# Optimization experiments

Measured on AMD Instinct MI355X. Metric: run time of the kernel, lower is better.

Reference implementation:

```python
import jax, jax.numpy as jnp
import numpy as np

B = 256          # batch
T = 256          # block_size (tril mask requires seq_len == 256)
E = 384          # n_embed
H = 6            # n_head
HS = E // H      # head_size = 64
EPS = 1e-5       # torch LayerNorm default


def layernorm(x, g, b):
    m = x.mean(-1, keepdims=True)
    v = x.var(-1, keepdims=True)  # population variance, matches torch LN
    return (x - m) * jax.lax.rsqrt(v + EPS) * g + b


def setup_inputs() -> dict:
    key = jax.random.key(0)
    ks = jax.random.split(key, 8)
    s = lambda i, shape: jax.random.normal(ks[i], shape, jnp.float32) * 0.02
    return {
        "x": jax.random.normal(ks[0], (B, T, E), jnp.float32),
        # per-head Q/K/V linears (bias=False) packed along output dim: [E, H*HS]
        "Wq": s(1, (E, E)), "Wk": s(2, (E, E)), "Wv": s(3, (E, E)),
        "Wo": s(4, (E, E)), "bo": jnp.zeros((E,), jnp.float32),
        "W1": s(5, (E, 4 * E)), "b1": jnp.zeros((4 * E,), jnp.float32),
        "W2": s(6, (4 * E, E)), "b2": jnp.zeros((E,), jnp.float32),
        "g1": jnp.ones((E,), jnp.float32), "be1": jnp.zeros((E,), jnp.float32),
        "g2": jnp.ones((E,), jnp.float32), "be2": jnp.zeros((E,), jnp.float32),
    }


def reference(x, Wq, Wk, Wv, Wo, bo, W1, b1, W2, b2, g1, be1, g2, be2):
    # Block.forward: ffwd(ln2(sa(ln1(x)) + x)) + x   (dropout = identity at eval)
    h = layernorm(x, g1, be1)                                  # [B,T,E]
    q = (h @ Wq).reshape(B, T, H, HS)
    k = (h @ Wk).reshape(B, T, H, HS)
    v = (h @ Wv).reshape(B, T, H, HS)
    wei = jnp.einsum('bqhd,bkhd->bhqk', q, k) * (HS ** -0.5)   # [B,H,T,T]
    mask = jnp.tril(jnp.ones((T, T), dtype=bool))
    wei = jnp.where(mask, wei, -jnp.inf)
    wei = jax.nn.softmax(wei, axis=-1)
    attn = jnp.einsum('bhqk,bkhd->bqhd', wei, v).reshape(B, T, E)
    sa = attn @ Wo + bo                                        # output projection
    y = sa + x                                                 # residual 1
    h2 = layernorm(y, g2, be2)
    ff = jax.nn.relu(h2 @ W1 + b1) @ W2 + b2                   # FFN
    return ff + x                                              # residual 2 (to x!)
```

## Files before the change

### kernel.cpp

```cpp
#include <hip/hip_runtime.h>
#include <hip/hip_bf16.h>

typedef unsigned short bfu;
typedef __attribute__((ext_vector_type(8))) short short8;
typedef __attribute__((ext_vector_type(4))) float f32x4;

__device__ __forceinline__ bfu f2bf(float f) {
  return __builtin_bit_cast(bfu, __float2bfloat16(f));
}

__device__ __forceinline__ void gld16(const void* g, void* l) {
  __builtin_amdgcn_global_load_lds(
      (const __attribute__((address_space(1))) void*)g,
      (__attribute__((address_space(3))) void*)l, 16, 0, 0);
}

__device__ __forceinline__ int swz8(int row, int sl) {
  return (row << 7) + (((sl ^ (row & 7)) & 7) << 4);
}

__device__ __forceinline__ int swz(int row, int slot) {
  const int unit = row >> 1;
  const int s8 = ((row & 1) << 2) | slot;
  return (unit << 7) + (((s8 ^ unit) & 7) << 4) + ((s8 >> 3) << 7);
}
__device__ __forceinline__ void unswz(int p, int& row, int& colel) {
  const int unit = p >> 7;
  const int s8 = ((p >> 4) & 7) ^ (unit & 7);
  row = (unit << 1) | (s8 >> 2);
  colel = (s8 & 3) << 3;
}

__global__ void transpose_all(const float* __restrict__ Wq, const float* __restrict__ Wk,
                              const float* __restrict__ Wv, const float* __restrict__ Wo,
                              const float* __restrict__ W1, const float* __restrict__ W2,
                              bfu* __restrict__ wqkvT, bfu* __restrict__ woT,
                              bfu* __restrict__ w1T, bfu* __restrict__ w2T) {
  int idx = blockIdx.x * 256 + threadIdx.x;
  if (idx < 4 * 147456) {
    int r = idx / 147456, i = idx - r * 147456;
    int k = i / 384, n = i - k * 384;
    const float* W = r == 0 ? Wq : r == 1 ? Wk : r == 2 ? Wv : Wo;
    bfu* dst = r < 3 ? wqkvT + r * 147456 : woT;
    dst[n * 384 + k] = f2bf(W[i]);
  } else if (idx < 4 * 147456 + 589824) {
    int i = idx - 4 * 147456;
    int k = i / 1536, n = i - k * 1536;
    w1T[n * 384 + k] = f2bf(W1[i]);
  } else if (idx < 4 * 147456 + 2 * 589824) {
    int i = idx - 4 * 147456 - 589824;
    int k = i / 384, n = i - k * 384;
    w2T[(size_t)n * 1536 + k] = f2bf(W2[i]);
  }
}

__launch_bounds__(256)
__global__ void ln_kernel(const float* __restrict__ in, const float* __restrict__ g,
                          const float* __restrict__ be, bfu* __restrict__ out) {
  const int wv = threadIdx.x >> 6, ln = threadIdx.x & 63;
  const size_t row = (size_t)blockIdx.x * 4 + wv;
  const float* p = in + row * 384;
  float v[6], s = 0.f, ss = 0.f;
#pragma unroll
  for (int i = 0; i < 6; i++) { v[i] = p[i * 64 + ln]; s += v[i]; ss += v[i] * v[i]; }
#pragma unroll
  for (int m = 1; m < 64; m <<= 1) { s += __shfl_xor(s, m); ss += __shfl_xor(ss, m); }
  const float mean = s * (1.f / 384.f);
  const float rs = rsqrtf(ss * (1.f / 384.f) - mean * mean + 1e-5f);
  bfu* q = out + row * 384;
#pragma unroll
  for (int i = 0; i < 6; i++) {
    const int c = i * 64 + ln;
    q[c] = f2bf((v[i] - mean) * rs * g[c] + be[c]);
  }
}

template <int BIAS, int RELU, int RES, int OUTBF>
__launch_bounds__(512)
__global__ void gemm8p(const bfu* __restrict__ A, const bfu* __restrict__ Bt,
                       const float* __restrict__ bias, const float* __restrict__ res,
                       void* __restrict__ Cout, int N, int K, int ntn) {
  __shared__ bfu sm[3][384 * 64];
  const int tid = threadIdx.x;
  const int wv = tid >> 6, ln = tid & 63;
  const int cpx = gridDim.x >> 3;
  const int wg = (blockIdx.x & 7) * cpx + (blockIdx.x >> 3);
  const int bm = wg / ntn, bn = wg - bm * ntn;
  const int m0 = bm << 8, n0 = bn << 7;
  const int wr = wv >> 1, wc = wv & 1;
  const int fr = ln & 15, fslot = ln >> 4;

  f32x4 acc[4][4];
#pragma unroll
  for (int i = 0; i < 4; i++)
#pragma unroll
    for (int j = 0; j < 4; j++) acc[i][j] = f32x4{0.f, 0.f, 0.f, 0.f};

  const int lr = ln >> 3;
  const int lslot = (ln & 7) ^ lr;

  auto stage = [&](int s, int kt) {
    char* smA = (char*)sm[s];
    char* smB = smA + 256 * 64 * 2;
    const int kcol = (kt << 6) + (lslot << 3);
#pragma unroll
    for (int i = 0; i < 4; ++i) {
      const int c = (wv << 2) + i;
      gld16(A + (size_t)(m0 + (c << 3) + lr) * K + kcol, smA + (c << 10));
    }
#pragma unroll
    for (int i = 0; i < 2; ++i) {
      const int c = (wv << 1) + i;
      gld16(Bt + (size_t)(n0 + (c << 3) + lr) * K + kcol, smB + (c << 10));
    }
  };

  const int nk = K >> 6;
  stage(0, 0);
  if (nk > 1) {
    stage(1, 1);
    asm volatile("s_waitcnt vmcnt(6)" ::: "memory");
  } else {
    asm volatile("s_waitcnt vmcnt(0)" ::: "memory");
  }
  __builtin_amdgcn_s_barrier();

  for (int kt = 0; kt < nk; ++kt) {
    const int s = kt - (kt / 3) * 3;
    const char* smA = (const char*)sm[s];
    const char* smB = smA + 256 * 64 * 2;
    if (kt + 2 < nk) stage((kt + 2) - ((kt + 2) / 3) * 3, kt + 2);
    short8 af[4], bf[4];
#pragma unroll
    for (int mi = 0; mi < 4; mi++)
      af[mi] = *(const short8*)(smA + swz8(wr * 64 + mi * 16 + fr, fslot));
#pragma unroll
    for (int ni = 0; ni < 4; ni++)
      bf[ni] = *(const short8*)(smB + swz8(wc * 64 + ni * 16 + fr, fslot));
    __builtin_amdgcn_s_barrier();
    asm volatile("s_waitcnt lgkmcnt(0)" ::: "memory");
    __builtin_amdgcn_sched_barrier(0);
    __builtin_amdgcn_s_setprio(1);
#pragma unroll
    for (int mi = 0; mi < 4; mi++)
#pragma unroll
      for (int ni = 0; ni < 4; ni++)
        acc[mi][ni] = __builtin_amdgcn_mfma_f32_16x16x32_bf16(af[mi], bf[ni], acc[mi][ni], 0, 0, 0);
    __builtin_amdgcn_s_setprio(0);
    __builtin_amdgcn_s_barrier();
#pragma unroll
    for (int mi = 0; mi < 4; mi++)
      af[mi] = *(const short8*)(smA + swz8(wr * 64 + mi * 16 + fr, 4 + fslot));
#pragma unroll
    for (int ni = 0; ni < 4; ni++)
      bf[ni] = *(const short8*)(smB + swz8(wc * 64 + ni * 16 + fr, 4 + fslot));
    __builtin_amdgcn_s_barrier();
    asm volatile("s_waitcnt lgkmcnt(0)" ::: "memory");
    __builtin_amdgcn_sched_barrier(0);
    __builtin_amdgcn_s_setprio(1);
#pragma unroll
    for (int mi = 0; mi < 4; mi++)
#pragma unroll
      for (int ni = 0; ni < 4; ni++)
        acc[mi][ni] = __builtin_amdgcn_mfma_f32_16x16x32_bf16(af[mi], bf[ni], acc[mi][ni], 0, 0, 0);
    __builtin_amdgcn_s_setprio(0);
    if (kt + 2 < nk)      asm volatile("s_waitcnt vmcnt(6)" ::: "memory");
    else if (kt + 1 < nk) asm volatile("s_waitcnt vmcnt(0)" ::: "memory");
    __builtin_amdgcn_s_barrier();
  }

  const int rq = (ln >> 4) << 2;
#pragma unroll
  for (int mi = 0; mi < 4; mi++) {
#pragma unroll
    for (int ni = 0; ni < 4; ni++) {
      const int row = m0 + wr * 64 + mi * 16 + rq;
      const int col = n0 + wc * 64 + ni * 16 + fr;
      float bv = 0.f;
      if (BIAS) bv = bias[col];
#pragma unroll
      for (int r = 0; r < 4; r++) {
        float v = acc[mi][ni][r] + bv;
        if (RELU) v = fmaxf(v, 0.f);
        const size_t idx = (size_t)(row + r) * N + col;
        if (RES) v += res[idx];
        if (OUTBF) ((bfu*)Cout)[idx] = f2bf(v);
        else       ((float*)Cout)[idx] = v;
      }
    }
  }
}

template <int LN>
__launch_bounds__(512)
__global__ void row_gemm(const bfu* __restrict__ A, const bfu* __restrict__ Bt,
                         const float* __restrict__ bias, const float* __restrict__ res,
                         const float* __restrict__ g, const float* __restrict__ be,
                         void* __restrict__ Cout, int K) {
  __shared__ bfu a_sm[4][128 * 32];
  __shared__ bfu b_sm[4][384 * 32];
  __shared__ float lnp[4][128][2];
  const int tid = threadIdx.x;
  const int wv = tid >> 6, ln = tid & 63;
  const int wr = wv >> 2, wc = wv & 3;
  const int fr = ln & 15, fslot = ln >> 4;
  const int m0 = blockIdx.x << 7;

  f32x4 acc[4][6];
#pragma unroll
  for (int i = 0; i < 4; i++)
#pragma unroll
    for (int j = 0; j < 6; j++) acc[i][j] = f32x4{0.f, 0.f, 0.f, 0.f};

  auto stage = [&](int buf, int kt) {
#pragma unroll
    for (int i = 0; i < 4; ++i) {
      const int c = wv * 4 + i;
      const int cc = (c < 8) ? c : (c - 8);
      const int p = cc * 1024 + (ln << 4);
      int r, colel;
      unswz(p, r, colel);
      const int col = kt * 32 + colel;
      if (c < 8)
        gld16(A + (size_t)(m0 + r) * K + col, (char*)a_sm[buf] + cc * 1024);
      else
        gld16(Bt + (size_t)r * K + col, (char*)b_sm[buf] + cc * 1024);
    }
  };

  const int nk = K >> 5;
#pragma unroll
  for (int i = 0; i < 3; ++i)
    if (i < nk) stage(i, i);

  for (int kt = 0; kt < nk; ++kt) {
    const int rem = nk - 1 - kt;
    if (rem >= 2)      asm volatile("s_waitcnt vmcnt(8)" ::: "memory");
    else if (rem == 1) asm volatile("s_waitcnt vmcnt(4)" ::: "memory");
    else               asm volatile("s_waitcnt vmcnt(0)" ::: "memory");
    __builtin_amdgcn_s_barrier();
    __builtin_amdgcn_sched_barrier(0);
    if (kt + 3 < nk) stage((kt + 3) & 3, kt + 3);
    const int cb = kt & 3;
    short8 af[4], bfr[6];
#pragma unroll
    for (int mi = 0; mi < 4; mi++)
      af[mi] = *(const short8*)((const char*)a_sm[cb] + swz(wr * 64 + mi * 16 + fr, fslot));
#pragma unroll
    for (int ni = 0; ni < 6; ni++)
      bfr[ni] = *(const short8*)((const char*)b_sm[cb] + swz(wc * 96 + ni * 16 + fr, fslot));
    __builtin_amdgcn_s_setprio(1);
#pragma unroll
    for (int mi = 0; mi < 4; mi++)
#pragma unroll
      for (int ni = 0; ni < 6; ni++)
        acc[mi][ni] = __builtin_amdgcn_mfma_f32_16x16x32_bf16(af[mi], bfr[ni], acc[mi][ni], 0, 0, 0);
    __builtin_amdgcn_s_setprio(0);
  }

  const int rq = (ln >> 4) << 2;
#pragma unroll
  for (int mi = 0; mi < 4; mi++) {
    const int row = wr * 64 + mi * 16 + rq;
#pragma unroll
    for (int ni = 0; ni < 6; ni++) {
      const int col = wc * 96 + ni * 16 + fr;
      const float bv = bias[col];
#pragma unroll
      for (int r = 0; r < 4; r++)
        acc[mi][ni][r] += bv + res[(size_t)(m0 + row + r) * 384 + col];
    }
  }

  if (LN) {
#pragma unroll
    for (int mi = 0; mi < 4; mi++) {
      float s[4] = {0.f, 0.f, 0.f, 0.f}, ss[4] = {0.f, 0.f, 0.f, 0.f};
#pragma unroll
      for (int ni = 0; ni < 6; ni++)
#pragma unroll
        for (int r = 0; r < 4; r++) {
          const float v = acc[mi][ni][r];
          s[r] += v; ss[r] += v * v;
        }
#pragma unroll
      for (int m = 1; m < 16; m <<= 1)
#pragma unroll
        for (int r = 0; r < 4; r++) {
          s[r] += __shfl_xor(s[r], m);
          ss[r] += __shfl_xor(ss[r], m);
        }
      if (fr == 0) {
#pragma unroll
        for (int r = 0; r < 4; r++) {
          lnp[wc][wr * 64 + mi * 16 + rq + r][0] = s[r];
          lnp[wc][wr * 64 + mi * 16 + rq + r][1] = ss[r];
        }
      }
    }
    __syncthreads();
#pragma unroll
    for (int mi = 0; mi < 4; mi++) {
#pragma unroll
      for (int r = 0; r < 4; r++) {
        const int row = wr * 64 + mi * 16 + rq + r;
        const float sm = lnp[0][row][0] + lnp[1][row][0] + lnp[2][row][0] + lnp[3][row][0];
        const float sq = lnp[0][row][1] + lnp[1][row][1] + lnp[2][row][1] + lnp[3][row][1];
        const float mean = sm * (1.f / 384.f);
        const float rs = rsqrtf(sq * (1.f / 384.f) - mean * mean + 1e-5f);
#pragma unroll
        for (int ni = 0; ni < 6; ni++) {
          const int col = wc * 96 + ni * 16 + fr;
          ((bfu*)Cout)[(size_t)(m0 + row) * 384 + col] =
              f2bf((acc[mi][ni][r] - mean) * rs * g[col] + be[col]);
        }
      }
    }
  } else {
#pragma unroll
    for (int mi = 0; mi < 4; mi++) {
      const int row = wr * 64 + mi * 16 + rq;
#pragma unroll
      for (int ni = 0; ni < 6; ni++) {
        const int col = wc * 96 + ni * 16 + fr;
#pragma unroll
        for (int r = 0; r < 4; r++)
          ((float*)Cout)[(size_t)(m0 + row + r) * 384 + col] = acc[mi][ni][r];
      }
    }
  }
}

#define KPAD 72
#define VPAD 264
#define PPAD 264

__launch_bounds__(512)
__global__ void attn_kernel(const bfu* __restrict__ qkv, bfu* __restrict__ ob) {
  __shared__ bfu k_sm[256 * KPAD];
  __shared__ bfu vt_sm[64 * VPAD];
  __shared__ bfu p_sm[8 * 16 * PPAD];
  const int b = blockIdx.x / 6, h = blockIdx.x - b * 6;
  const int tid = threadIdx.x;
  const int wv = tid >> 6, ln = tid & 63;
  const int fr = ln & 15, fc = (ln >> 4) << 3;
  const size_t inbase = (size_t)b * 256 * 1152 + h * 64;
  const bfu* qb = qkv + inbase;
  const bfu* kb = qkv + inbase + 384;
  const bfu* vb = qkv + inbase + 768;
  const size_t obase = (size_t)b * 256 * 384 + h * 64;

  {
    const int row = tid >> 1;
    const int dh = (tid & 1) << 5;
    const bfu* kg = kb + (size_t)row * 1152 + dh;
    const bfu* vg = vb + (size_t)row * 1152 + dh;
#pragma unroll
    for (int i = 0; i < 4; i++) {
      short8 t8 = *(const short8*)(kg + i * 8);
      *(short8*)&k_sm[row * KPAD + dh + i * 8] = t8;
      short8 v8 = *(const short8*)(vg + i * 8);
#pragma unroll
      for (int j = 0; j < 8; j++)
        vt_sm[(dh + i * 8 + j) * VPAD + row] = (bfu)v8[j];
    }
  }
  __syncthreads();

  bfu* pw = &p_sm[wv * 16 * PPAD];
  const int rq = (ln >> 4) << 2;

#pragma unroll
  for (int si = 0; si < 2; ++si) {
    const int s = si ? (15 - wv) : wv;
    const int qr0 = s << 4;
    const int nf = s + 1;
    short8 aq[2];
#pragma unroll
    for (int dc = 0; dc < 2; dc++)
      aq[dc] = *(const short8*)(qb + (size_t)(qr0 + fr) * 1152 + dc * 32 + fc);

    f32x4 sacc[16];
#pragma unroll
    for (int f = 0; f < 16; f++) sacc[f] = f32x4{0.f, 0.f, 0.f, 0.f};
#pragma unroll
    for (int f = 0; f < 16; f++) if (f < nf) {
#pragma unroll
      for (int dc = 0; dc < 2; dc++) {
        short8 kf = *(const short8*)&k_sm[(f * 16 + fr) * KPAD + dc * 32 + fc];
        sacc[f] = __builtin_amdgcn_mfma_f32_16x16x32_bf16(aq[dc], kf, sacc[f], 0, 0, 0);
      }
    }
    float mr[4] = {-3e38f, -3e38f, -3e38f, -3e38f};
#pragma unroll
    for (int f = 0; f < 16; f++) if (f < nf) {
#pragma unroll
      for (int r = 0; r < 4; r++) {
        float sv = sacc[f][r] * 0.125f;
        if (f * 16 + fr > qr0 + rq + r) sv = -3e38f;
        sacc[f][r] = sv;
        mr[r] = fmaxf(mr[r], sv);
      }
    }
#pragma unroll
    for (int msk = 1; msk < 16; msk <<= 1) {
#pragma unroll
      for (int r = 0; r < 4; r++) mr[r] = fmaxf(mr[r], __shfl_xor(mr[r], msk));
    }
    float ls[4] = {0.f, 0.f, 0.f, 0.f};
#pragma unroll
    for (int f = 0; f < 16; f++) if (f < nf) {
#pragma unroll
      for (int r = 0; r < 4; r++) {
        float p = __expf(sacc[f][r] - mr[r]);
        sacc[f][r] = p;
        ls[r] += p;
      }
    }
#pragma unroll
    for (int msk = 1; msk < 16; msk <<= 1) {
#pragma unroll
      for (int r = 0; r < 4; r++) ls[r] += __shfl_xor(ls[r], msk);
    }
#pragma unroll
    for (int f = 0; f < 16; f++) if (f < nf) {
#pragma unroll
      for (int r = 0; r < 4; r++)
        pw[(rq + r) * PPAD + f * 16 + fr] = f2bf(sacc[f][r]);
    }
    if (nf & 1) {
#pragma unroll
      for (int r = 0; r < 4; r++) pw[(rq + r) * PPAD + nf * 16 + fr] = 0;
    }
    f32x4 oc[4];
#pragma unroll
    for (int n = 0; n < 4; n++) oc[n] = f32x4{0.f, 0.f, 0.f, 0.f};
    const int kcs = (nf + 1) >> 1;
#pragma unroll
    for (int kc = 0; kc < 8; ++kc) if (kc < kcs) {
      short8 pa = *(const short8*)&pw[fr * PPAD + kc * 32 + fc];
#pragma unroll
      for (int n = 0; n < 4; n++) {
        short8 vf = *(const short8*)&vt_sm[(n * 16 + fr) * VPAD + kc * 32 + fc];
        oc[n] = __builtin_amdgcn_mfma_f32_16x16x32_bf16(pa, vf, oc[n], 0, 0, 0);
      }
    }
    float inv[4];
#pragma unroll
    for (int r = 0; r < 4; r++) inv[r] = 1.f / ls[r];
#pragma unroll
    for (int n = 0; n < 4; n++) {
#pragma unroll
      for (int r = 0; r < 4; r++)
        ob[obase + (size_t)(qr0 + rq + r) * 384 + n * 16 + fr] = f2bf(oc[n][r] * inv[r]);
    }
  }
}

extern "C" void kernel_launch(void* const* d_in, const int* in_sizes, int n_in,
                              void* d_out, int out_size, void* d_ws, size_t ws_size,
                              hipStream_t stream) {
  const float* x   = (const float*)d_in[0];
  const float* Wq  = (const float*)d_in[1];
  const float* Wk  = (const float*)d_in[2];
  const float* Wv  = (const float*)d_in[3];
  const float* Wo  = (const float*)d_in[4];
  const float* bo  = (const float*)d_in[5];
  const float* W1  = (const float*)d_in[6];
  const float* b1  = (const float*)d_in[7];
  const float* W2  = (const float*)d_in[8];
  const float* b2  = (const float*)d_in[9];
  const float* g1  = (const float*)d_in[10];
  const float* be1 = (const float*)d_in[11];
  const float* g2  = (const float*)d_in[12];
  const float* be2 = (const float*)d_in[13];
  float* out = (float*)d_out;
  char* ws = (char*)d_ws;

  bfu* wqkvT = (bfu*)(ws + 0);
  bfu* woT   = (bfu*)(ws + 884736);
  bfu* w1T   = (bfu*)(ws + 1179648);
  bfu* w2T   = (bfu*)(ws + 2359296);
  char* H    = ws + 3538944;
  char* BIG  = H + 50331648;
  bfu* hb    = (bfu*)BIG;
  bfu* qkvb  = (bfu*)(BIG + 50331648);
  bfu* attnb = (bfu*)BIG;
  bfu* h2b   = (bfu*)H;
  bfu* ab    = (bfu*)BIG;

  transpose_all<<<6912, 256, 0, stream>>>(Wq, Wk, Wv, Wo, W1, W2, wqkvT, woT, w1T, w2T);

  ln_kernel<<<16384, 256, 0, stream>>>(x, g1, be1, hb);

  gemm8p<0, 0, 0, 1><<<2304, 512, 0, stream>>>(hb, wqkvT, nullptr, nullptr, qkvb, 1152, 384, 9);

  attn_kernel<<<1536, 512, 0, stream>>>(qkvb, attnb);

  row_gemm<1><<<512, 512, 0, stream>>>(attnb, woT, bo, x, g2, be2, h2b, 384);

  gemm8p<1, 1, 0, 1><<<3072, 512, 0, stream>>>(h2b, w1T, b1, nullptr, ab, 1536, 384, 12);

  gemm8p<1, 0, 1, 0><<<768, 512, 0, stream>>>(ab, w2T, b2, x, out, 384, 1536, 3);
}
```

Measured before the change: 509.6 us.

## Replace GEMM with templated four-phase double-buffered kernel and retune tiles

Replaces the triple-buffered 256x128 GEMM with a templated kernel whose tile size is set by per-wave fragment counts (WM, WN). It double-buffers LDS and splits each K step into four phases that interleave the next tile's A and B global-to-LDS loads with MFMA work. Each launch gets its own tile shape (256x192 for QKV, 256x256 for FFN1, 128x384 for FFN2), cutting grid sizes and reusing each staged A tile across more columns. The cost is more accumulator registers, which may lower occupancy, and a shallower prefetch depth. The unused non-LN path of row_gemm is also removed.

```diff
diff --git a/kernel.cpp b/kernel.cpp
--- a/kernel.cpp
+++ b/kernel.cpp
@@ -75,107 +75,106 @@
   }
 }
 
-template <int BIAS, int RELU, int RES, int OUTBF>
+template <int WM, int WN, int BIAS, int RELU, int RES, int OUTBF>
 __launch_bounds__(512)
-__global__ void gemm8p(const bfu* __restrict__ A, const bfu* __restrict__ Bt,
-                       const float* __restrict__ bias, const float* __restrict__ res,
-                       void* __restrict__ Cout, int N, int K, int ntn) {
-  __shared__ bfu sm[3][384 * 64];
+__global__ void gemm_ph(const bfu* __restrict__ A, const bfu* __restrict__ Bt,
+                        const float* __restrict__ bias, const float* __restrict__ res,
+                        void* __restrict__ Cout, int N, int K, int ntn) {
+  constexpr int BM = WM * 32;
+  constexpr int BN = WN * 64;
+  constexpr int ACH = BM / 64;
+  constexpr int BCH = BN / 64;
+  __shared__ bfu sm[2][(BM + BN) * 64];
   const int tid = threadIdx.x;
   const int wv = tid >> 6, ln = tid & 63;
   const int cpx = gridDim.x >> 3;
   const int wg = (blockIdx.x & 7) * cpx + (blockIdx.x >> 3);
   const int bm = wg / ntn, bn = wg - bm * ntn;
-  const int m0 = bm << 8, n0 = bn << 7;
-  const int wr = wv >> 1, wc = wv & 1;
+  const int m0 = bm * BM, n0 = bn * BN;
+  const int wr = wv >> 2, wc = wv & 3;
   const int fr = ln & 15, fslot = ln >> 4;
-
-  f32x4 acc[4][4];
-#pragma unroll
-  for (int i = 0; i < 4; i++)
-#pragma unroll
-    for (int j = 0; j < 4; j++) acc[i][j] = f32x4{0.f, 0.f, 0.f, 0.f};
-
-  const int lr = ln >> 3;
-  const int lslot = (ln & 7) ^ lr;
-
-  auto stage = [&](int s, int kt) {
+  const int lr = ln >> 3, lsl = (ln & 7) ^ lr;
+
+  f32x4 acc[WM][WN];
+#pragma unroll
+  for (int i = 0; i < WM; i++)
+#pragma unroll
+    for (int j = 0; j < WN; j++) acc[i][j] = f32x4{0.f, 0.f, 0.f, 0.f};
+
+  auto stageA = [&](int s, int kt) {
     char* smA = (char*)sm[s];
-    char* smB = smA + 256 * 64 * 2;
-    const int kcol = (kt << 6) + (lslot << 3);
-#pragma unroll
-    for (int i = 0; i < 4; ++i) {
-      const int c = (wv << 2) + i;
-      gld16(A + (size_t)(m0 + (c << 3) + lr) * K + kcol, smA + (c << 10));
-    }
-#pragma unroll
-    for (int i = 0; i < 2; ++i) {
-      const int c = (wv << 1) + i;
-      gld16(Bt + (size_t)(n0 + (c << 3) + lr) * K + kcol, smB + (c << 10));
+    const int col = (kt << 6) + (lsl << 3);
+#pragma unroll
+    for (int i = 0; i < ACH; ++i) {
+      const int c = wv * ACH + i;
+      gld16(A + (size_t)(m0 + (c << 3) + lr) * K + col, smA + (c << 10));
     }
   };
+  auto stageB = [&](int s, int kt) {
+    char* smB = (char*)sm[s] + BM * 128;
+    const int col = (kt << 6) + (lsl << 3);
+#pragma unroll
+    for (int i = 0; i < BCH; ++i) {
+      const int c = wv * BCH + i;
+      gld16(Bt + (size_t)(n0 + (c << 3) + lr) * K + col, smB + (c << 10));
+    }
+  };
 
   const int nk = K >> 6;
-  stage(0, 0);
-  if (nk > 1) {
-    stage(1, 1);
-    asm volatile("s_waitcnt vmcnt(6)" ::: "memory");
-  } else {
-    asm volatile("s_waitcnt vmcnt(0)" ::: "memory");
-  }
+  stageA(0, 0);
+  stageB(0, 0);
+  asm volatile("s_waitcnt vmcnt(0)" ::: "memory");
   __builtin_amdgcn_s_barrier();
 
   for (int kt = 0; kt < nk; ++kt) {
-    const int s = kt - (kt / 3) * 3;
-    const char* smA = (const char*)sm[s];
-    const char* smB = smA + 256 * 64 * 2;
-    if (kt + 2 < nk) stage((kt + 2) - ((kt + 2) / 3) * 3, kt + 2);
-    short8 af[4], bf[4];
-#pragma unroll
-    for (int mi = 0; mi < 4; mi++)
-      af[mi] = *(const short8*)(smA + swz8(wr * 64 + mi * 16 + fr, fslot));
-#pragma unroll
-    for (int ni = 0; ni < 4; ni++)
-      bf[ni] = *(const short8*)(smB + swz8(wc * 64 + ni * 16 + fr, fslot));
-    __builtin_amdgcn_s_barrier();
-    asm volatile("s_waitcnt lgkmcnt(0)" ::: "memory");
-    __builtin_amdgcn_sched_barrier(0);
-    __builtin_amdgcn_s_setprio(1);
-#pragma unroll
-    for (int mi = 0; mi < 4; mi++)
-#pragma unroll
-      for (int ni = 0; ni < 4; ni++)
-        acc[mi][ni] = __builtin_amdgcn_mfma_f32_16x16x32_bf16(af[mi], bf[ni], acc[mi][ni], 0, 0, 0);
-    __builtin_amdgcn_s_setprio(0);
-    __builtin_amdgcn_s_barrier();
-#pragma unroll
-    for (int mi = 0; mi < 4; mi++)
-      af[mi] = *(const short8*)(smA + swz8(wr * 64 + mi * 16 + fr, 4 + fslot));
-#pragma unroll
-    for (int ni = 0; ni < 4; ni++)
-      bf[ni] = *(const short8*)(smB + swz8(wc * 64 + ni * 16 + fr, 4 + fslot));
-    __builtin_amdgcn_s_barrier();
-    asm volatile("s_waitcnt lgkmcnt(0)" ::: "memory");
-    __builtin_amdgcn_sched_barrier(0);
-    __builtin_amdgcn_s_setprio(1);
-#pragma unroll
-    for (int mi = 0; mi < 4; mi++)
-#pragma unroll
-      for (int ni = 0; ni < 4; ni++)
-        acc[mi][ni] = __builtin_amdgcn_mfma_f32_16x16x32_bf16(af[mi], bf[ni], acc[mi][ni], 0, 0, 0);
-    __builtin_amdgcn_s_setprio(0);
-    if (kt + 2 < nk)      asm volatile("s_waitcnt vmcnt(6)" ::: "memory");
-    else if (kt + 1 < nk) asm volatile("s_waitcnt vmcnt(0)" ::: "memory");
-    __builtin_amdgcn_s_barrier();
+    const int cur = kt & 1;
+    const char* smA = (const char*)sm[cur];
+    const char* smB = smA + BM * 128;
+    short8 bf[2][WN];
+#pragma unroll
+    for (int ph = 0; ph < 4; ++ph) {
+      const int mh = ph >> 1, ks = ph & 1;
+      short8 af[WM / 2];
+#pragma unroll
+      for (int i = 0; i < WM / 2; ++i)
+        af[i] = *(const short8*)(smA +
+            swz8(wr * (WM * 16) + (mh * (WM / 2) + i) * 16 + fr, ks * 4 + fslot));
+      if (mh == 0) {
+#pragma unroll
+        for (int ni = 0; ni < WN; ++ni)
+          bf[ks][ni] = *(const short8*)(smB +
+              swz8(wc * (WN * 16) + ni * 16 + fr, ks * 4 + fslot));
+      }
+      if (kt + 1 < nk) {
+        if (ph == 0) stageA(cur ^ 1, kt + 1);
+        if (ph == 1) stageB(cur ^ 1, kt + 1);
+      }
+      __builtin_amdgcn_s_barrier();
+      asm volatile("s_waitcnt lgkmcnt(0)" ::: "memory");
+      __builtin_amdgcn_sched_barrier(0);
+      __builtin_amdgcn_s_setprio(1);
+#pragma unroll
+      for (int i = 0; i < WM / 2; ++i)
+#pragma unroll
+        for (int ni = 0; ni < WN; ++ni)
+          acc[mh * (WM / 2) + i][ni] = __builtin_amdgcn_mfma_f32_16x16x32_bf16(
+              af[i], bf[ks][ni], acc[mh * (WM / 2) + i][ni], 0, 0, 0);
+      __builtin_amdgcn_s_setprio(0);
+      __builtin_amdgcn_s_barrier();
+    }
+    if (kt + 1 < nk) {
+      asm volatile("s_waitcnt vmcnt(0)" ::: "memory");
+      __builtin_amdgcn_s_barrier();
+    }
   }
 
   const int rq = (ln >> 4) << 2;
 #pragma unroll
-  for (int mi = 0; mi < 4; mi++) {
-#pragma unroll
-    for (int ni = 0; ni < 4; ni++) {
-      const int row = m0 + wr * 64 + mi * 16 + rq;
-      const int col = n0 + wc * 64 + ni * 16 + fr;
+  for (int mi = 0; mi < WM; mi++) {
+#pragma unroll
+    for (int ni = 0; ni < WN; ni++) {
+      const int row = m0 + wr * (WM * 16) + mi * 16 + rq;
+      const int col = n0 + wc * (WN * 16) + ni * 16 + fr;
       float bv = 0.f;
       if (BIAS) bv = bias[col];
 #pragma unroll
@@ -191,7 +190,6 @@
   }
 }
 
-template <int LN>
 __launch_bounds__(512)
 __global__ void row_gemm(const bfu* __restrict__ A, const bfu* __restrict__ Bt,
                          const float* __restrict__ bias, const float* __restrict__ res,
@@ -272,60 +270,46 @@
     }
   }
 
-  if (LN) {
-#pragma unroll
-    for (int mi = 0; mi < 4; mi++) {
-      float s[4] = {0.f, 0.f, 0.f, 0.f}, ss[4] = {0.f, 0.f, 0.f, 0.f};
-#pragma unroll
-      for (int ni = 0; ni < 6; ni++)
-#pragma unroll
-        for (int r = 0; r < 4; r++) {
-          const float v = acc[mi][ni][r];
-          s[r] += v; ss[r] += v * v;
-        }
-#pragma unroll
-      for (int m = 1; m < 16; m <<= 1)
-#pragma unroll
-        for (int r = 0; r < 4; r++) {
-          s[r] += __shfl_xor(s[r], m);
-          ss[r] += __shfl_xor(ss[r], m);
-        }
-      if (fr == 0) {
-#pragma unroll
-        for (int r = 0; r < 4; r++) {
-          lnp[wc][wr * 64 + mi * 16 + rq + r][0] = s[r];
-          lnp[wc][wr * 64 + mi * 16 + rq + r][1] = ss[r];
-        }
-      }
-    }
-    __syncthreads();
-#pragma unroll
-    for (int mi = 0; mi < 4; mi++) {
-#pragma unroll
-      for (int r = 0; r < 4; r++) {
-        const int row = wr * 64 + mi * 16 + rq + r;
-        const float sm = lnp[0][row][0] + lnp[1][row][0] + lnp[2][row][0] + lnp[3][row][0];
-        const float sq = lnp[0][row][1] + lnp[1][row][1] + lnp[2][row][1] + lnp[3][row][1];
-        const float mean = sm * (1.f / 384.f);
-        const float rs = rsqrtf(sq * (1.f / 384.f) - mean * mean + 1e-5f);
-#pragma unroll
-        for (int ni = 0; ni < 6; ni++) {
-          const int col = wc * 96 + ni * 16 + fr;
-          ((bfu*)Cout)[(size_t)(m0 + row) * 384 + col] =
-              f2bf((acc[mi][ni][r] - mean) * rs * g[col] + be[col]);
-        }
-      }
-    }
-  } else {
-#pragma unroll
-    for (int mi = 0; mi < 4; mi++) {
-      const int row = wr * 64 + mi * 16 + rq;
+#pragma unroll
+  for (int mi = 0; mi < 4; mi++) {
+    float s[4] = {0.f, 0.f, 0.f, 0.f}, ss[4] = {0.f, 0.f, 0.f, 0.f};
+#pragma unroll
+    for (int ni = 0; ni < 6; ni++)
+#pragma unroll
+      for (int r = 0; r < 4; r++) {
+        const float v = acc[mi][ni][r];
+        s[r] += v; ss[r] += v * v;
+      }
+#pragma unroll
+    for (int m = 1; m < 16; m <<= 1)
+#pragma unroll
+      for (int r = 0; r < 4; r++) {
+        s[r] += __shfl_xor(s[r], m);
+        ss[r] += __shfl_xor(ss[r], m);
+      }
+    if (fr == 0) {
+#pragma unroll
+      for (int r = 0; r < 4; r++) {
+        lnp[wc][wr * 64 + mi * 16 + rq + r][0] = s[r];
+        lnp[wc][wr * 64 + mi * 16 + rq + r][1] = ss[r];
+      }
+    }
+  }
+  __syncthreads();
+#pragma unroll
+  for (int mi = 0; mi < 4; mi++) {
+#pragma unroll
+    for (int r = 0; r < 4; r++) {
+      const int row = wr * 64 + mi * 16 + rq + r;
+      const float sm = lnp[0][row][0] + lnp[1][row][0] + lnp[2][row][0] + lnp[3][row][0];
+      const float sq = lnp[0][row][1] + lnp[1][row][1] + lnp[2][row][1] + lnp[3][row][1];
+      const float mean = sm * (1.f / 384.f);
+      const float rs = rsqrtf(sq * (1.f / 384.f) - mean * mean + 1e-5f);
 #pragma unroll
       for (int ni = 0; ni < 6; ni++) {
         const int col = wc * 96 + ni * 16 + fr;
-#pragma unroll
-        for (int r = 0; r < 4; r++)
-          ((float*)Cout)[(size_t)(m0 + row + r) * 384 + col] = acc[mi][ni][r];
+        ((bfu*)Cout)[(size_t)(m0 + row) * 384 + col] =
+            f2bf((acc[mi][ni][r] - mean) * rs * g[col] + be[col]);
       }
     }
   }
@@ -493,13 +477,13 @@
 
   ln_kernel<<<16384, 256, 0, stream>>>(x, g1, be1, hb);
 
-  gemm8p<0, 0, 0, 1><<<2304, 512, 0, stream>>>(hb, wqkvT, nullptr, nullptr, qkvb, 1152, 384, 9);
+  gemm_ph<8, 3, 0, 0, 0, 1><<<1536, 512, 0, stream>>>(hb, wqkvT, nullptr, nullptr, qkvb, 1152, 384, 6);
 
   attn_kernel<<<1536, 512, 0, stream>>>(qkvb, attnb);
 
-  row_gemm<1><<<512, 512, 0, stream>>>(attnb, woT, bo, x, g2, be2, h2b, 384);
-
-  gemm8p<1, 1, 0, 1><<<3072, 512, 0, stream>>>(h2b, w1T, b1, nullptr, ab, 1536, 384, 12);
-
-  gemm8p<1, 0, 1, 0><<<768, 512, 0, stream>>>(ab, w2T, b2, x, out, 384, 1536, 3);
-}
+  row_gemm<<<512, 512, 0, stream>>>(attnb, woT, bo, x, g2, be2, h2b, 384);
+
+  gemm_ph<8, 4, 1, 1, 0, 1><<<1536, 512, 0, stream>>>(h2b, w1T, b1, nullptr, ab, 1536, 384, 6);
+
+  gemm_ph<4, 6, 1, 0, 1, 0><<<512, 512, 0, stream>>>(ab, w2T, b2, x, out, 384, 1536, 1);
+}
```

After: 493.5 us. -3.2%, faster.
